# Optimization experiments

Hardware: AMD Instinct MI355X
Metric: run time of the kernel (lower is better)

Reference implementation:

```python
import jax, jax.numpy as jnp
import numpy as np

N, NS, B = 4096, 256, 2
X, Y, Z = 128, 128, 16
R = 4                      # compress_ratio per spatial axis
C, NC, H = 128, 20, 8      # feat dim, num classes, heads
DH = C // H
EPS = 1e-5


def setup_inputs() -> dict:
    rng = np.random.default_rng(0)
    gx_n, gy_n, gz_n = X // R, Y // R, Z // R
    # pick NS//B unique super-voxel cells per batch element
    cells = np.stack([rng.choice(gx_n * gy_n * gz_n, NS // B, replace=False) for _ in range(B)])
    gx = cells // (gy_n * gz_n)
    rem = cells % (gy_n * gz_n)
    gy, gz = rem // gz_n, rem % gz_n
    bidx = np.repeat(np.arange(B), NS // B)
    sv = np.stack([bidx, gx.ravel(), gy.ravel(), gz.ravel()], axis=1)  # [NS,4]
    per = N // NS  # 16 voxels per super-voxel, distinct offsets in the 4x4x4 cell
    offs = np.argsort(rng.random((NS, R * R * R)), axis=1)[:, :per]
    dx, dy, dz = offs // (R * R), (offs // R) % R, offs % R
    vox = np.stack([
        np.repeat(sv[:, 0], per),
        (sv[:, 1, None] * R + dx).ravel(),
        (sv[:, 2, None] * R + dy).ravel(),
        (sv[:, 3, None] * R + dz).ravel()], axis=1).astype(np.int32)

    ks = jax.random.split(jax.random.key(0), 12)
    p = lambda k, shape, s=0.02: jax.random.normal(k, shape, jnp.float32) * s
    return dict(
        indices=jnp.asarray(vox),
        features=jax.random.normal(ks[0], (N, C), jnp.float32),
        cw1=p(ks[1], (C, C)), cb1=jnp.zeros(C), cg1=jnp.ones(C), cbe1=jnp.zeros(C),
        cw2=p(ks[2], (C, C)), cb2=jnp.zeros(C),
        pw1=p(ks[3], (3, 64)), pb1=jnp.zeros(64), pg1=jnp.ones(64), pbe1=jnp.zeros(64),
        pw2=p(ks[4], (64, 1)), pb2=jnp.zeros(1),
        wq=p(ks[5], (C, C)), bq=jnp.zeros(C),
        wk=p(ks[6], (C, C)), bk=jnp.zeros(C),
        wv=p(ks[7], (C, C)), bv=jnp.zeros(C),
        wo=p(ks[8], (C, C)), bo=jnp.zeros(C),
        ln_g=jnp.ones(C), ln_b=jnp.zeros(C),
        seg_w=p(ks[9], (3, 3, 3, C, NC)), seg_b=jnp.zeros(NC),
    )


def _bn(x, g, b):  # BatchNorm1d, training-mode batch statistics
    mu = x.mean(0)
    var = x.var(0)
    return (x - mu) * jax.lax.rsqrt(var + EPS) * g + b


def reference(indices, features, cw1, cb1, cg1, cbe1, cw2, cb2,
              pw1, pb1, pg1, pbe1, pw2, pb2,
              wq, bq, wk, bk, wv, bv, wo, bo, ln_g, ln_b, seg_w, seg_b):
    ratio = jnp.array([1, R, R, R], dtype=indices.dtype)
    comp = indices // ratio                                  # [N,4] super-voxel coord
    unq, inv = jnp.unique(comp, axis=0, size=NS, return_inverse=True)
    # scatter-add softmax(features) over super-voxels
    cf = jax.ops.segment_sum(jax.nn.softmax(features, axis=1), inv, num_segments=NS)
    h = jax.nn.relu(_bn(cf @ cw1 + cb1, cg1, cbe1)) @ cw2 + cb2      # [NS,C]
    # pairwise relative-position bias: tiny MLP over [N*NS,3]
    pos = (indices[:, None, 1:] - unq[None, :, 1:]).astype(jnp.float32).reshape(N * NS, 3)
    pbias = (jax.nn.relu(_bn(pos @ pw1 + pb1, pg1, pbe1)) @ pw2 + pb2).reshape(N, NS)
    # multi-head cross attention: voxels query super-voxels, bias added to scores
    q = (features @ wq + bq).reshape(N, H, DH)
    k = (h @ wk + bk).reshape(NS, H, DH)
    v = (h @ wv + bv).reshape(NS, H, DH)
    scores = jnp.einsum('nhd,shd->hns', q, k) / np.float32(np.sqrt(DH)) + pbias[None]
    attn = jax.nn.softmax(scores, axis=-1)                   # [H,N,NS]
    ctx = jnp.einsum('hns,shd->nhd', attn, v).reshape(N, C) @ wo + bo
    y = features + ctx                                       # residual + LayerNorm sublayer
    mu = y.mean(-1, keepdims=True)
    var = y.var(-1, keepdims=True)
    y = (y - mu) * jax.lax.rsqrt(var + EPS) * ln_g + ln_b
    # SubMConv3d(128->20, k=3, pad=1): dense scatter -> conv -> gather at active sites
    grid = jnp.zeros((B, X, Y, Z, C), jnp.float32).at[
        indices[:, 0], indices[:, 1], indices[:, 2], indices[:, 3]].set(y)
    out = jax.lax.conv_general_dilated(
        grid, seg_w, (1, 1, 1), 'SAME',
        dimension_numbers=('NDHWC', 'DHWIO', 'NDHWC')) + seg_b
    return out[indices[:, 0], indices[:, 1], indices[:, 2], indices[:, 3]]  # [N,NC]
```

## Files before the change

### kernel.cpp

```cpp
#include <hip/hip_runtime.h>

typedef unsigned short ushort_t;

#define NVOX 4096
#define NSV  256
#define XD   128
#define YD   128
#define ZD   16
#define CD   128
#define NCD  20
#define HD   8
#define DHD  16
#define MAPN 524288
#define EPSF 1e-5f

#define OF_FEAT 0
#define OF_CW1  524288
#define OF_CB1  540672
#define OF_CG1  540800
#define OF_CBE1 540928
#define OF_CW2  541056
#define OF_CB2  557440
#define OF_PW1  557568
#define OF_PB1  557760
#define OF_PG1  557824
#define OF_PBE1 557888
#define OF_PW2  557952
#define OF_PB2  558016
#define OF_WQ   558080
#define OF_BQ   574464
#define OF_WK   574592
#define OF_BK   590976
#define OF_WV   591104
#define OF_BV   607488
#define OF_WO   607616
#define OF_BO   624000
#define OF_LNG  624128
#define OF_LNB  624256
#define OF_SEGW 624384
#define OF_SEGB 693504
#define ARENA_N 693568
#define TOTCVT  624341

__device__ __forceinline__ float bf2f(const ushort_t* p){
  return __uint_as_float(((unsigned)(*p)) << 16);
}
__device__ __forceinline__ ushort_t f2bf(float f){
  unsigned u = __float_as_uint(f);
  u += 0x7fffu + ((u >> 16) & 1u);
  return (ushort_t)(u >> 16);
}
__device__ __forceinline__ float unlo(unsigned u){ return __uint_as_float(u << 16); }
__device__ __forceinline__ float unhi(unsigned u){ return __uint_as_float(u & 0xffff0000u); }

struct SrcPtrs { const void* p[25]; };

__device__ const int g_cnt[25] = {524288,16384,128,128,128,16384,128,192,64,64,64,64,1,
                                  16384,128,16384,128,16384,128,16384,128,128,128,0,20};
__device__ const int g_off[25] = {OF_FEAT,OF_CW1,OF_CB1,OF_CG1,OF_CBE1,OF_CW2,OF_CB2,
                                  OF_PW1,OF_PB1,OF_PG1,OF_PBE1,OF_PW2,OF_PB2,
                                  OF_WQ,OF_BQ,OF_WK,OF_BK,OF_WV,OF_BV,OF_WO,OF_BO,
                                  OF_LNG,OF_LNB,OF_SEGW,OF_SEGB};

__device__ __forceinline__ float ldi(const void* p, int off, int fl){
  return fl ? bf2f((const ushort_t*)p + off) : ((const float*)p)[off];
}

struct SPREP {
  float frows[16][CD];
  float qpart[2][16][CD];
  float part[8][CD];
  float cfs[CD];
  float gpart[8][CD];
};
union __align__(16) UPREP { SPREP sv; int smom[18]; };

__global__ __launch_bounds__(512) void kprep(SrcPtrs sp, const int* idx, int* flag,
    float* arena, float* wt, int* map, float* afold_g, float* scfold_g,
    float* qb, float* t1T)
{
  __shared__ UPREP sm;
  __shared__ int sm_flag;
  int t = threadIdx.x, b = blockIdx.x;
  if (t < 64){
    const ushort_t* f16 = (const ushort_t*)sp.p[0];
    unsigned u = f16[2*t];
    int e = (u >> 7) & 0xFF;
    int sane = (u == 0 || (e >= 90 && e <= 150)) ? 1 : 0;
    unsigned long long bl = __ballot(sane);
    if (t == 0) sm_flag = (__popcll(bl) >= 48) ? 1 : 0;
  }
  __syncthreads();
  const int fl = sm_flag;

  if (b < 255){
    int gid = b*512 + t;
    const int GS = 255*512;
    if (gid == 0) *flag = fl;
    for (int k=gid; k<MAPN; k+=GS) map[k] = -1;
    for (int el=gid; el<TOTCVT; el+=GS){
      int s=0, rem=el;
      while (rem >= g_cnt[s]){ rem -= g_cnt[s]; ++s; }
      arena[g_off[s]+rem] = ldi(sp.p[s], rem, fl);
    }
    for (int k=gid; k<27*NCD*CD; k+=GS){
      int nb = k/(NCD*CD); int rem = k - nb*(NCD*CD); int o = rem/CD, i = rem - o*CD;
      wt[k] = ldi(sp.p[23], nb*(CD*NCD) + i*NCD + o, fl);
    }
  } else if (b < 511){
    int sv = b - 255;
    int rb = sv*16;
    if (fl){
      const uint2* fsrc = (const uint2*)((const ushort_t*)sp.p[0] + (size_t)rb*CD);
      uint2 u = fsrc[t];
      float* dst = &sm.sv.frows[t>>5][(t&31)*4];
      dst[0]=unlo(u.x); dst[1]=unhi(u.x); dst[2]=unlo(u.y); dst[3]=unhi(u.y);
    } else {
      const float4* fsrc = (const float4*)((const float*)sp.p[0] + (size_t)rb*CD);
      ((float4*)sm.sv.frows)[t] = fsrc[t];
    }
    __syncthreads();
    {
      int c8 = (t&15)*8, r = (t>>4)&15, kh = t>>8;
      int i0 = kh*64;
      float acc[8] = {0.f,0.f,0.f,0.f,0.f,0.f,0.f,0.f};
      if (fl){
        const ushort_t* wqp = (const ushort_t*)sp.p[13];
        #pragma unroll 4
        for (int i=i0; i<i0+64; ++i){
          uint4 w4 = *(const uint4*)(wqp + (size_t)i*CD + c8);
          float fr = sm.sv.frows[r][i];
          acc[0] += unlo(w4.x)*fr; acc[1] += unhi(w4.x)*fr;
          acc[2] += unlo(w4.y)*fr; acc[3] += unhi(w4.y)*fr;
          acc[4] += unlo(w4.z)*fr; acc[5] += unhi(w4.z)*fr;
          acc[6] += unlo(w4.w)*fr; acc[7] += unhi(w4.w)*fr;
        }
      } else {
        const float* wqp = (const float*)sp.p[13];
        #pragma unroll 4
        for (int i=i0; i<i0+64; ++i){
          float4 wa = *(const float4*)(wqp + (size_t)i*CD + c8);
          float4 wb = *(const float4*)(wqp + (size_t)i*CD + c8 + 4);
          float fr = sm.sv.frows[r][i];
          acc[0]+=wa.x*fr; acc[1]+=wa.y*fr; acc[2]+=wa.z*fr; acc[3]+=wa.w*fr;
          acc[4]+=wb.x*fr; acc[5]+=wb.y*fr; acc[6]+=wb.z*fr; acc[7]+=wb.w*fr;
        }
      }
      #pragma unroll
      for (int j=0;j<8;++j) sm.sv.qpart[kh][r][c8+j] = acc[j];
    }
    __syncthreads();
    for (int e = t; e < 16*CD; e += 512){
      int r = e>>7, c = e&127;
      qb[(size_t)(rb+r)*CD + c] = sm.sv.qpart[0][r][c] + sm.sv.qpart[1][r][c]
                                + ldi(sp.p[14], c, fl);
    }
    {
      int w = t>>6, l = t&63;
      float a0 = 0.f, a1 = 0.f;
      #pragma unroll
      for (int k=0;k<2;++k){
        int r = w*2 + k;
        float f0 = sm.sv.frows[r][l];
        float f1 = sm.sv.frows[r][l+64];
        float m = fmaxf(f0,f1);
        #pragma unroll
        for (int o=32;o;o>>=1) m = fmaxf(m, __shfl_xor(m,o,64));
        float e0 = __expf(f0-m), e1 = __expf(f1-m);
        float ssum = e0+e1;
        #pragma unroll
        for (int o=32;o;o>>=1) ssum += __shfl_xor(ssum,o,64);
        float inv = 1.f/ssum;
        a0 += e0*inv; a1 += e1*inv;
      }
      sm.sv.part[w][l] = a0; sm.sv.part[w][l+64] = a1;
    }
    __syncthreads();
    if (t < CD){
      float s = 0.f;
      #pragma unroll
      for (int w=0;w<8;++w) s += sm.sv.part[w][t];
      sm.sv.cfs[t] = s;
    }
    __syncthreads();
    {
      int c2 = (t&63)*2, kg = t>>6;
      int i0 = kg*16;
      float a0 = 0.f, a1 = 0.f;
      if (fl){
        const ushort_t* W = (const ushort_t*)sp.p[1];
        #pragma unroll 4
        for (int i=i0; i<i0+16; ++i){
          unsigned w = *(const unsigned*)(W + (size_t)i*CD + c2);
          float cfv = sm.sv.cfs[i];
          a0 += unlo(w)*cfv; a1 += unhi(w)*cfv;
        }
      } else {
        const float* W = (const float*)sp.p[1];
        #pragma unroll 4
        for (int i=i0; i<i0+16; ++i){
          float2 w = *(const float2*)(W + (size_t)i*CD + c2);
          float cfv = sm.sv.cfs[i];
          a0 += w.x*cfv; a1 += w.y*cfv;
        }
      }
      sm.sv.gpart[kg][c2] = a0; sm.sv.gpart[kg][c2+1] = a1;
    }
    __syncthreads();
    if (t < CD){
      float s = 0.f;
      #pragma unroll
      for (int kg=0;kg<8;++kg) s += sm.sv.gpart[kg][t];
      t1T[(size_t)t*NSV + sv] = s + ldi(sp.p[2], t, fl);
    }
  } else {
    if (t < 18) sm.smom[t] = 0;
    __syncthreads();
    {
      int sacc[9] = {0,0,0,0,0,0,0,0,0};
      for (int v = t; v < NVOX; v += 512){
        int4 q = ((const int4*)idx)[v];
        sacc[0]+=q.y; sacc[1]+=q.z; sacc[2]+=q.w;
        sacc[3]+=q.y*q.y; sacc[4]+=q.z*q.z; sacc[5]+=q.w*q.w;
        sacc[6]+=q.y*q.z; sacc[7]+=q.y*q.w; sacc[8]+=q.z*q.w;
      }
      int um[9] = {0,0,0,0,0,0,0,0,0};
      if (t < 256){
        int4 q = ((const int4*)idx)[t*16];
        int gx=q.y>>2, gy=q.z>>2, gz=q.w>>2;
        um[0]=gx; um[1]=gy; um[2]=gz;
        um[3]=gx*gx; um[4]=gy*gy; um[5]=gz*gz;
        um[6]=gx*gy; um[7]=gx*gz; um[8]=gy*gz;
      }
      int lane = t & 63;
      #pragma unroll
      for (int i=0;i<9;++i){
        int s = sacc[i];
        int u = um[i];
        #pragma unroll
        for (int o=32;o;o>>=1){
          s += __shfl_xor(s, o, 64);
          u += __shfl_xor(u, o, 64);
        }
        if (lane == 0){
          if (s) atomicAdd(&sm.smom[9+i], s);
          if (u) atomicAdd(&sm.smom[i], u);
        }
      }
    }
    __syncthreads();
    if (t < 64){
      int* smom = sm.smom;
      double U1[3]={(double)smom[0],(double)smom[1],(double)smom[2]};
      double S1[3]={(double)smom[9],(double)smom[10],(double)smom[11]};
      double Uxx[3][3], Sxx[3][3];
      Uxx[0][0]=smom[3]; Uxx[1][1]=smom[4]; Uxx[2][2]=smom[5];
      Uxx[0][1]=Uxx[1][0]=smom[6]; Uxx[0][2]=Uxx[2][0]=smom[7]; Uxx[1][2]=Uxx[2][1]=smom[8];
      Sxx[0][0]=smom[12]; Sxx[1][1]=smom[13]; Sxx[2][2]=smom[14];
      Sxx[0][1]=Sxx[1][0]=smom[15]; Sxx[0][2]=Sxx[2][0]=smom[16]; Sxx[1][2]=Sxx[2][1]=smom[17];
      double M1[3], M2[3][3];
      for (int a=0;a<3;++a) M1[a] = 256.0*S1[a] - 4096.0*U1[a];
      for (int a=0;a<3;++a)
        for (int b2=0;b2<3;++b2)
          M2[a][b2] = 256.0*Sxx[a][b2] - S1[a]*U1[b2] - S1[b2]*U1[a] + 4096.0*Uxx[a][b2];
      double wv_[3]={(double)ldi(sp.p[7],t,fl),(double)ldi(sp.p[7],64+t,fl),(double)ldi(sp.p[7],128+t,fl)};
      double bj=(double)ldi(sp.p[8],t,fl), gj=(double)ldi(sp.p[9],t,fl), bej=(double)ldi(sp.p[10],t,fl);
      double Mw=0.0, wMw=0.0;
      for (int a=0;a<3;++a){
        Mw += M1[a]*wv_[a];
        for (int b2=0;b2<3;++b2) wMw += wv_[a]*M2[a][b2]*wv_[b2];
      }
      const double NM = 1048576.0;
      double mean = Mw/NM + bj;
      double Ey2  = wMw/NM + 2.0*bj*Mw/NM + bj*bj;
      double var  = Ey2 - mean*mean;
      double scale = gj / sqrt(var + 1e-5);
      afold_g[t]      = (float)(wv_[0]*scale);
      afold_g[64+t]   = (float)(wv_[1]*scale);
      afold_g[128+t]  = (float)(wv_[2]*scale);
      scfold_g[t]     = (float)(bj*scale + bej - mean*scale);
    }
  }
}

__global__ __launch_bounds__(256) void k6_fused(const float* t1T, const float* A,
    const int* idx, int* map, float* kb, float* vb){
  __shared__ float row[CD];
  __shared__ float cpar[2][CD];
  __shared__ float hrow[CD];
  int t = threadIdx.x;
  int role = blockIdx.x >> 8, s = blockIdx.x & 255;
  if (role == 0 && t >= 128 && t < 144){
    int v = s*16 + (t-128);
    int4 q = ((const int4*)idx)[v];
    map[((q.x*XD + q.y)*YD + q.z)*ZD + q.w] = v;
  }
  if (t < CD){
    const float4* col = (const float4*)(t1T + (size_t)t*NSV);
    float sum=0.f, sq=0.f;
    #pragma unroll 8
    for (int i=0;i<NSV/4;++i){
      float4 v = col[i];
      sum += v.x+v.y+v.z+v.w;
      sq  += v.x*v.x+v.y*v.y+v.z*v.z+v.w*v.w;
    }
    float mean = sum*(1.f/256.f);
    float var  = sq*(1.f/256.f) - mean*mean;
    float scv = A[OF_CG1+t]*rsqrtf(var+EPSF);
    float shv = A[OF_CBE1+t] - mean*scv;
    row[t] = fmaxf(t1T[(size_t)t*NSV + s]*scv + shv, 0.f);
  }
  __syncthreads();
  int c = t&127, half = t>>7;
  {
    const float* W = A + OF_CW2;
    float acc = 0.f;
    #pragma unroll 8
    for (int i=half*64;i<half*64+64;++i) acc += row[i]*W[i*CD+c];
    cpar[half][c] = acc;
  }
  __syncthreads();
  if (t < CD) hrow[t] = cpar[0][t]+cpar[1][t]+A[OF_CB2+t];
  __syncthreads();
  {
    const float* W = role ? (A+OF_WV) : (A+OF_WK);
    float acc = 0.f;
    #pragma unroll 8
    for (int i=half*64;i<half*64+64;++i) acc += hrow[i]*W[i*CD+c];
    cpar[half][c] = acc;
  }
  __syncthreads();
  if (t < CD){
    float v = cpar[0][t]+cpar[1][t] + (role ? A[OF_BV+t] : A[OF_BK+t]);
    if (role) vb[(size_t)s*CD+t] = v; else kb[(size_t)s*CD+t] = v;
  }
}

#define CGRP(row,hh) (((hh) + ((row)>>1)) & 3)

__global__ __launch_bounds__(256, 6) void k9_attn(
    const float* A, const int* idx, const float* afold_g, const float* scfold_g,
    const float* kb, const float* vb, const float* qb, float* yb)
{
  __shared__ __align__(16) float q4s[4][CD];
  __shared__ __align__(16) float scf[NSV][16];
  __shared__ __align__(16) float ctxT[CD*4];
  __shared__ float cpart[4][4][64];
  __shared__ __align__(16) float e4T[64][4];
  __shared__ float saf[3][64];
  __shared__ float ssc[64];
  __shared__ float w2s[64];
  __shared__ float rinv[32];
  int t = threadIdx.x;
  int n0 = blockIdx.x*4;
  if (t < 128) ((float4*)q4s)[t] = ((const float4*)(qb + (size_t)n0*CD))[t];
  if (t < 64){
    saf[0][t] = afold_g[t]; saf[1][t] = afold_g[64+t]; saf[2][t] = afold_g[128+t];
    ssc[t] = scfold_g[t]; w2s[t] = A[OF_PW2+t];
  }
  __syncthreads();
  {
    int g = t>>6, j = t&63;
    float xv = (float)idx[4*(n0+g)+1];
    float yv = (float)idx[4*(n0+g)+2];
    float zv = (float)idx[4*(n0+g)+3];
    e4T[j][g] = saf[0][j]*xv + saf[1][j]*yv + saf[2][j]*zv;
  }
  __syncthreads();
  float pbv[4];
  {
    int4 q0 = ((const int4*)idx)[t*16];
    float uxf = (float)(q0.y>>2), uyf = (float)(q0.z>>2), uzf = (float)(q0.w>>2);
    float pb2v = A[OF_PB2];
    #pragma unroll
    for (int g=0;g<4;++g) pbv[g] = pb2v;
    #pragma unroll 2
    for (int j=0;j<64;++j){
      float dj = ssc[j] - (saf[0][j]*uxf + saf[1][j]*uyf + saf[2][j]*uzf);
      float wj = w2s[j];
      float4 ea = *(const float4*)&e4T[j][0];
      pbv[0] += fmaxf(ea.x+dj,0.f)*wj; pbv[1] += fmaxf(ea.y+dj,0.f)*wj;
      pbv[2] += fmaxf(ea.z+dj,0.f)*wj; pbv[3] += fmaxf(ea.w+dj,0.f)*wj;
    }
  }
  const float4* krow = (const float4*)(kb + (size_t)t*CD);
  #pragma unroll
  for (int p=0;p<2;++p){
    {
      #pragma unroll
      for (int hh=0; hh<4; ++hh){
        int h = p*4 + hh;
        float4 k0 = krow[h*4+0], k1 = krow[h*4+1], k2 = krow[h*4+2], k3 = krow[h*4+3];
        float pr[4];
        #pragma unroll
        for (int g=0; g<4; ++g){
          const float* qg = &q4s[g][h*DHD];
          float dot = qg[0]*k0.x + qg[1]*k0.y + qg[2]*k0.z + qg[3]*k0.w
                    + qg[4]*k1.x + qg[5]*k1.y + qg[6]*k1.z + qg[7]*k1.w
                    + qg[8]*k2.x + qg[9]*k2.y + qg[10]*k2.z + qg[11]*k2.w
                    + qg[12]*k3.x + qg[13]*k3.y + qg[14]*k3.z + qg[15]*k3.w;
          pr[g] = __expf(dot*0.25f + pbv[g]);
        }
        *(float4*)&scf[t][CGRP(t,hh)*4] = make_float4(pr[0],pr[1],pr[2],pr[3]);
      }
    }
    __syncthreads();
    {
      int g = t>>6, lane = t&63;
      #pragma unroll
      for (int hh=0; hh<4; ++hh){
        float s0 = 0.f;
        #pragma unroll
        for (int k=0;k<4;++k){
          int r = lane + 64*k;
          s0 += scf[r][CGRP(r,hh)*4 + g];
        }
        #pragma unroll
        for (int o=32;o;o>>=1) s0 += __shfl_xor(s0,o,64);
        if (lane==0) rinv[g*8 + p*4 + hh] = 1.f/s0;
      }
    }
    {
      int q = t>>6, c = t&63;
      int hh = c>>4;
      const float* vcol = vb + p*64 + c;
      float a0=0.f, a1=0.f, a2=0.f, a3=0.f;
      #pragma unroll 4
      for (int s=q*64; s<q*64+64; ++s){
        float v = vcol[(size_t)s*CD];
        float4 pv = *(const float4*)&scf[s][CGRP(s,hh)*4];
        a0 += pv.x*v; a1 += pv.y*v; a2 += pv.z*v; a3 += pv.w*v;
      }
      cpart[q][0][c]=a0; cpart[q][1][c]=a1; cpart[q][2][c]=a2; cpart[q][3][c]=a3;
    }
    __syncthreads();
    {
      int gsel = t>>6, c = t&63;
      int ch = p*64 + c, h = ch>>4;
      ctxT[ch*4+gsel] = (cpart[0][gsel][c]+cpart[1][gsel][c]
                        +cpart[2][gsel][c]+cpart[3][gsel][c]) * rinv[gsel*8+h];
    }
  }
  __syncthreads();
  {
    int half=t>>7, c=t&127;
    const float* wo = A + OF_WO;
    float acc[4]={0.f,0.f,0.f,0.f};
    #pragma unroll 4
    for (int i=half*64;i<half*64+64;++i){
      float wv = wo[i*CD+c];
      float4 r = *(const float4*)&ctxT[i*4];
      acc[0]+=r.x*wv; acc[1]+=r.y*wv; acc[2]+=r.z*wv; acc[3]+=r.w*wv;
    }
    #pragma unroll
    for (int g=0;g<4;++g) cpart[(c>>6)*2 + half][g][c&63] = acc[g];
  }
  __syncthreads();
  if (t < CD){
    float bov = A[OF_BO+t];
    int chi = t>>6, cl = t&63;
    #pragma unroll
    for (int g=0;g<4;++g)
      ctxT[t*4+g] = cpart[chi*2+0][g][cl] + cpart[chi*2+1][g][cl] + bov
                  + A[OF_FEAT + (size_t)(n0+g)*CD + t];
  }
  __syncthreads();
  {
    int g = t>>6, lane = t&63;
    float x0 = ctxT[lane*4+g], x1 = ctxT[(lane+64)*4+g];
    float s1 = x0+x1, s2 = x0*x0+x1*x1;
    #pragma unroll
    for (int o=32;o;o>>=1){ s1 += __shfl_xor(s1,o,64); s2 += __shfl_xor(s2,o,64); }
    float mean = s1*(1.f/128.f);
    float var  = s2*(1.f/128.f) - mean*mean;
    float rs = rsqrtf(var + EPSF);
    yb[(size_t)(n0+g)*CD + lane]    = (x0-mean)*rs*A[OF_LNG+lane]    + A[OF_LNB+lane];
    yb[(size_t)(n0+g)*CD + lane+64] = (x1-mean)*rs*A[OF_LNG+lane+64] + A[OF_LNB+lane+64];
  }
}

__global__ __launch_bounds__(256) void k10_conv(const int* idx, const int* map,
    const float* yb, const float* A, const float* wt, const int* flag, void* outv)
{
  __shared__ int sco4[8][4];
  __shared__ int jn[8][27];
  __shared__ float partial[4][8][NCD];
  int t = threadIdx.x;
  int p0 = blockIdx.x*8;
  if (t < 32) ((int*)sco4)[t] = idx[4*p0 + t];
  __syncthreads();
  if (t < 216){
    int v = t/27, nb = t - v*27;
    int kd = nb/9, kh = (nb/3)%3, kw = nb%3;
    int bb = sco4[v][0];
    int nx = sco4[v][1]+kd-1, ny = sco4[v][2]+kh-1, nz = sco4[v][3]+kw-1;
    int j = -1;
    if ((unsigned)nx < XD && (unsigned)ny < YD && (unsigned)nz < ZD)
      j = map[((bb*XD+nx)*YD+ny)*ZD+nz];
    jn[v][nb] = j;
  }
  __syncthreads();
  int w = t>>6, l = t&63;
  int og = l & 3, cg = l >> 2;
  int c0 = cg*8;
  float acc[8][5];
  #pragma unroll
  for (int v=0;v<8;++v)
    #pragma unroll
    for (int oo=0;oo<5;++oo) acc[v][oo]=0.f;
  for (int nb = w; nb < 27; nb += 4){
    const float* wbase = wt + (size_t)nb*NCD*CD + c0;
    float4 wreg[10];
    #pragma unroll
    for (int oo=0;oo<5;++oo){
      wreg[oo*2]   = *(const float4*)(wbase + (size_t)(og*5+oo)*CD);
      wreg[oo*2+1] = *(const float4*)(wbase + (size_t)(og*5+oo)*CD + 4);
    }
    #pragma unroll
    for (int v=0; v<8; ++v){
      int j = jn[v][nb];
      if (j < 0) continue;
      const float4* y4 = (const float4*)(yb + (size_t)j*CD + c0);
      float4 ya = y4[0], ybb = y4[1];
      #pragma unroll
      for (int oo=0;oo<5;++oo){
        float4 wa = wreg[oo*2], wb = wreg[oo*2+1];
        acc[v][oo] += ya.x*wa.x + ya.y*wa.y + ya.z*wa.z + ya.w*wa.w
                    + ybb.x*wb.x + ybb.y*wb.y + ybb.z*wb.z + ybb.w*wb.w;
      }
    }
  }
  #pragma unroll
  for (int v=0;v<8;++v)
    #pragma unroll
    for (int oo=0;oo<5;++oo){
      float s = acc[v][oo];
      s += __shfl_xor(s, 4, 64);
      s += __shfl_xor(s, 8, 64);
      s += __shfl_xor(s, 16, 64);
      s += __shfl_xor(s, 32, 64);
      if (cg == 0) partial[w][v][og*5+oo] = s;
    }
  __syncthreads();
  if (t < 160){
    int v = t/20, o = t - v*20;
    float s = partial[0][v][o]+partial[1][v][o]+partial[2][v][o]+partial[3][v][o]
            + A[OF_SEGB+o];
    if (*flag) ((ushort_t*)outv)[(size_t)(p0+v)*NCD + o] = f2bf(s);
    else       ((float*)outv)[(size_t)(p0+v)*NCD + o]   = s;
  }
}

extern "C" void kernel_launch(void* const* d_in, const int* in_sizes, int n_in,
                              void* d_out, int out_size, void* d_ws, size_t ws_size,
                              hipStream_t stream) {
  const int* idx = (const int*)d_in[0];

  char* w = (char*)d_ws;
  size_t off = 0;
  #define ALLOC(name, type, count) \
    type* name = (type*)(w + off); off += (((size_t)(count)*sizeof(type)) + 255) & ~(size_t)255;
  ALLOC(flag,   int,   64)
  ALLOC(arena,  float, ARENA_N)
  ALLOC(wt,     float, 27*NCD*CD)
  ALLOC(map,    int,   MAPN)
  ALLOC(afold,  float, 192)
  ALLOC(scfold, float, 64)
  ALLOC(t1T,    float, CD*NSV)
  ALLOC(kb,     float, NSV*CD)
  ALLOC(vbuf,   float, NSV*CD)
  ALLOC(qb,     float, NVOX*CD)
  ALLOC(yb,     float, NVOX*CD)
  #undef ALLOC
  (void)off; (void)ws_size; (void)n_in; (void)in_sizes; (void)out_size;

  SrcPtrs sp;
  for (int i=0;i<25;++i) sp.p[i] = d_in[i+1];

  kprep   <<<512, 512, 0, stream>>>(sp, idx, flag, arena, wt, map, afold, scfold, qb, t1T);
  k6_fused<<<NSV*2, 256, 0, stream>>>(t1T, arena, idx, map, kb, vbuf);
  k9_attn <<<NVOX/4, 256, 0, stream>>>(arena, idx, afold, scfold, kb, vbuf, qb, yb);
  k10_conv<<<NVOX/8, 256, 0, stream>>>(idx, map, yb, arena, wt, flag, d_out);
}
```

Before: 204.6 us.

## Process both head halves concurrently in attention kernel with 512 threads

The attention kernel now launches 512 threads per block, so the two head-halves that were handled in a sequential loop run at the same time. The scores buffer is duplicated per half, and the positional bias is computed once and stored in shared memory. The output-projection reduction is split four ways. The intent is more parallelism per block and fewer serial phases and barriers. In exchange it uses more shared memory per block, which may lower occupancy, and the launch_bounds of 512 with 6 blocks per SM may constrain registers.

After: 206.5 us. Within noise of the previous version (+0.9%).

```diff
diff --git a/kernel.cpp b/kernel.cpp
--- a/kernel.cpp
+++ b/kernel.cpp
@@ -338,15 +338,16 @@
 
 #define CGRP(row,hh) (((hh) + ((row)>>1)) & 3)
 
-__global__ __launch_bounds__(256, 6) void k9_attn(
+__global__ __launch_bounds__(512, 6) void k9_attn(
     const float* A, const int* idx, const float* afold_g, const float* scfold_g,
     const float* kb, const float* vb, const float* qb, float* yb)
 {
   __shared__ __align__(16) float q4s[4][CD];
-  __shared__ __align__(16) float scf[NSV][16];
+  __shared__ __align__(16) float scf[2][NSV][16];
   __shared__ __align__(16) float ctxT[CD*4];
-  __shared__ float cpart[4][4][64];
+  __shared__ __align__(16) float cbuf[2048];
   __shared__ __align__(16) float e4T[64][4];
+  __shared__ __align__(16) float pbias_s[NSV][4];
   __shared__ float saf[3][64];
   __shared__ float ssc[64];
   __shared__ float w2s[64];
@@ -354,12 +355,13 @@
   int t = threadIdx.x;
   int n0 = blockIdx.x*4;
   if (t < 128) ((float4*)q4s)[t] = ((const float4*)(qb + (size_t)n0*CD))[t];
-  if (t < 64){
-    saf[0][t] = afold_g[t]; saf[1][t] = afold_g[64+t]; saf[2][t] = afold_g[128+t];
-    ssc[t] = scfold_g[t]; w2s[t] = A[OF_PW2+t];
-  }
-  __syncthreads();
-  {
+  else if (t < 192){
+    int j = t - 128;
+    saf[0][j] = afold_g[j]; saf[1][j] = afold_g[64+j]; saf[2][j] = afold_g[128+j];
+    ssc[j] = scfold_g[j]; w2s[j] = A[OF_PW2+j];
+  }
+  __syncthreads();
+  if (t < 256){
     int g = t>>6, j = t&63;
     float xv = (float)idx[4*(n0+g)+1];
     float yv = (float)idx[4*(n0+g)+2];
@@ -367,11 +369,11 @@
     e4T[j][g] = saf[0][j]*xv + saf[1][j]*yv + saf[2][j]*zv;
   }
   __syncthreads();
-  float pbv[4];
-  {
+  if (t < 256){
     int4 q0 = ((const int4*)idx)[t*16];
     float uxf = (float)(q0.y>>2), uyf = (float)(q0.z>>2), uzf = (float)(q0.w>>2);
     float pb2v = A[OF_PB2];
+    float pbv[4];
     #pragma unroll
     for (int g=0;g<4;++g) pbv[g] = pb2v;
     #pragma unroll 2
@@ -382,90 +384,96 @@
       pbv[0] += fmaxf(ea.x+dj,0.f)*wj; pbv[1] += fmaxf(ea.y+dj,0.f)*wj;
       pbv[2] += fmaxf(ea.z+dj,0.f)*wj; pbv[3] += fmaxf(ea.w+dj,0.f)*wj;
     }
-  }
-  const float4* krow = (const float4*)(kb + (size_t)t*CD);
-  #pragma unroll
-  for (int p=0;p<2;++p){
-    {
-      #pragma unroll
-      for (int hh=0; hh<4; ++hh){
-        int h = p*4 + hh;
-        float4 k0 = krow[h*4+0], k1 = krow[h*4+1], k2 = krow[h*4+2], k3 = krow[h*4+3];
-        float pr[4];
-        #pragma unroll
-        for (int g=0; g<4; ++g){
-          const float* qg = &q4s[g][h*DHD];
-          float dot = qg[0]*k0.x + qg[1]*k0.y + qg[2]*k0.z + qg[3]*k0.w
-                    + qg[4]*k1.x + qg[5]*k1.y + qg[6]*k1.z + qg[7]*k1.w
-                    + qg[8]*k2.x + qg[9]*k2.y + qg[10]*k2.z + qg[11]*k2.w
-                    + qg[12]*k3.x + qg[13]*k3.y + qg[14]*k3.z + qg[15]*k3.w;
-          pr[g] = __expf(dot*0.25f + pbv[g]);
-        }
-        *(float4*)&scf[t][CGRP(t,hh)*4] = make_float4(pr[0],pr[1],pr[2],pr[3]);
-      }
-    }
-    __syncthreads();
-    {
-      int g = t>>6, lane = t&63;
-      #pragma unroll
-      for (int hh=0; hh<4; ++hh){
-        float s0 = 0.f;
-        #pragma unroll
-        for (int k=0;k<4;++k){
-          int r = lane + 64*k;
-          s0 += scf[r][CGRP(r,hh)*4 + g];
-        }
-        #pragma unroll
-        for (int o=32;o;o>>=1) s0 += __shfl_xor(s0,o,64);
-        if (lane==0) rinv[g*8 + p*4 + hh] = 1.f/s0;
-      }
-    }
-    {
-      int q = t>>6, c = t&63;
-      int hh = c>>4;
-      const float* vcol = vb + p*64 + c;
-      float a0=0.f, a1=0.f, a2=0.f, a3=0.f;
-      #pragma unroll 4
-      for (int s=q*64; s<q*64+64; ++s){
-        float v = vcol[(size_t)s*CD];
-        float4 pv = *(const float4*)&scf[s][CGRP(s,hh)*4];
-        a0 += pv.x*v; a1 += pv.y*v; a2 += pv.z*v; a3 += pv.w*v;
-      }
-      cpart[q][0][c]=a0; cpart[q][1][c]=a1; cpart[q][2][c]=a2; cpart[q][3][c]=a3;
-    }
-    __syncthreads();
-    {
-      int gsel = t>>6, c = t&63;
-      int ch = p*64 + c, h = ch>>4;
-      ctxT[ch*4+gsel] = (cpart[0][gsel][c]+cpart[1][gsel][c]
-                        +cpart[2][gsel][c]+cpart[3][gsel][c]) * rinv[gsel*8+h];
-    }
-  }
-  __syncthreads();
-  {
-    int half=t>>7, c=t&127;
+    *(float4*)&pbias_s[t][0] = make_float4(pbv[0],pbv[1],pbv[2],pbv[3]);
+  }
+  __syncthreads();
+  {
+    int p = t>>8, ts = t&255;
+    const float4* krow = (const float4*)(kb + (size_t)ts*CD);
+    float4 pb = *(const float4*)&pbias_s[ts][0];
+    #pragma unroll
+    for (int hh=0; hh<4; ++hh){
+      int h = p*4 + hh;
+      float4 k0 = krow[h*4+0], k1 = krow[h*4+1], k2 = krow[h*4+2], k3 = krow[h*4+3];
+      float pr[4];
+      #pragma unroll
+      for (int g=0; g<4; ++g){
+        const float* qg = &q4s[g][h*DHD];
+        float dot = qg[0]*k0.x + qg[1]*k0.y + qg[2]*k0.z + qg[3]*k0.w
+                  + qg[4]*k1.x + qg[5]*k1.y + qg[6]*k1.z + qg[7]*k1.w
+                  + qg[8]*k2.x + qg[9]*k2.y + qg[10]*k2.z + qg[11]*k2.w
+                  + qg[12]*k3.x + qg[13]*k3.y + qg[14]*k3.z + qg[15]*k3.w;
+        float pbg = (g==0)?pb.x:((g==1)?pb.y:((g==2)?pb.z:pb.w));
+        pr[g] = __expf(dot*0.25f + pbg);
+      }
+      *(float4*)&scf[p][ts][CGRP(ts,hh)*4] = make_float4(pr[0],pr[1],pr[2],pr[3]);
+    }
+  }
+  __syncthreads();
+  {
+    int w = t>>6, lane = t&63, p = w>>2, g = w&3;
+    #pragma unroll
+    for (int hh=0; hh<4; ++hh){
+      float s0 = 0.f;
+      #pragma unroll
+      for (int k=0;k<4;++k){
+        int r = lane + 64*k;
+        s0 += scf[p][r][CGRP(r,hh)*4 + g];
+      }
+      #pragma unroll
+      for (int o=32;o;o>>=1) s0 += __shfl_xor(s0,o,64);
+      if (lane==0) rinv[g*8 + p*4 + hh] = 1.f/s0;
+    }
+  }
+  {
+    int p = t>>8, ts = t&255, q = ts>>6, c = ts&63, hh = c>>4;
+    const float* vcol = vb + p*64 + c;
+    float a0=0.f, a1=0.f, a2=0.f, a3=0.f;
+    #pragma unroll 4
+    for (int s=q*64; s<q*64+64; ++s){
+      float v = vcol[(size_t)s*CD];
+      float4 pv = *(const float4*)&scf[p][s][CGRP(s,hh)*4];
+      a0 += pv.x*v; a1 += pv.y*v; a2 += pv.z*v; a3 += pv.w*v;
+    }
+    cbuf[p*1024 + q*256 + 0*64 + c] = a0;
+    cbuf[p*1024 + q*256 + 1*64 + c] = a1;
+    cbuf[p*1024 + q*256 + 2*64 + c] = a2;
+    cbuf[p*1024 + q*256 + 3*64 + c] = a3;
+  }
+  __syncthreads();
+  {
+    int gsel = t>>7, c = t&127;
+    int p = c>>6, cl = c&63, h = c>>4;
+    ctxT[c*4+gsel] = (cbuf[p*1024 +   0 + gsel*64 + cl]
+                     +cbuf[p*1024 + 256 + gsel*64 + cl]
+                     +cbuf[p*1024 + 512 + gsel*64 + cl]
+                     +cbuf[p*1024 + 768 + gsel*64 + cl]) * rinv[gsel*8+h];
+  }
+  __syncthreads();
+  {
+    int kq = t>>7, c = t&127;
     const float* wo = A + OF_WO;
     float acc[4]={0.f,0.f,0.f,0.f};
     #pragma unroll 4
-    for (int i=half*64;i<half*64+64;++i){
+    for (int i=kq*32; i<kq*32+32; ++i){
       float wv = wo[i*CD+c];
       float4 r = *(const float4*)&ctxT[i*4];
       acc[0]+=r.x*wv; acc[1]+=r.y*wv; acc[2]+=r.z*wv; acc[3]+=r.w*wv;
     }
     #pragma unroll
-    for (int g=0;g<4;++g) cpart[(c>>6)*2 + half][g][c&63] = acc[g];
+    for (int g=0;g<4;++g) cbuf[kq*512 + g*128 + c] = acc[g];
   }
   __syncthreads();
   if (t < CD){
     float bov = A[OF_BO+t];
-    int chi = t>>6, cl = t&63;
     #pragma unroll
     for (int g=0;g<4;++g)
-      ctxT[t*4+g] = cpart[chi*2+0][g][cl] + cpart[chi*2+1][g][cl] + bov
+      ctxT[t*4+g] = cbuf[g*128+t] + cbuf[512+g*128+t] + cbuf[1024+g*128+t]
+                  + cbuf[1536+g*128+t] + bov
                   + A[OF_FEAT + (size_t)(n0+g)*CD + t];
   }
   __syncthreads();
-  {
+  if (t < 256){
     int g = t>>6, lane = t&63;
     float x0 = ctxT[lane*4+g], x1 = ctxT[(lane+64)*4+g];
     float s1 = x0+x1, s2 = x0*x0+x1*x1;
@@ -579,6 +587,6 @@
 
   kprep   <<<512, 512, 0, stream>>>(sp, idx, flag, arena, wt, map, afold, scfold, qb, t1T);
   k6_fused<<<NSV*2, 256, 0, stream>>>(t1T, arena, idx, map, kb, vbuf);
-  k9_attn <<<NVOX/4, 256, 0, stream>>>(arena, idx, afold, scfold, kb, vbuf, qb, yb);
+  k9_attn <<<NVOX/4, 512, 0, stream>>>(arena, idx, afold, scfold, kb, vbuf, qb, yb);
   k10_conv<<<NVOX/8, 256, 0, stream>>>(idx, map, yb, arena, wt, flag, d_out);
 }
```
